# Performance work log

Hardware: AMD Instinct MI355X
Metric: run time of the kernel (lower is better)

Reference implementation:

```python
import jax, jax.numpy as jnp
import numpy as np

N_GROUPS = 8192
BETA = 0.99
EPS = 1e-12  # torch.nn.functional.normalize default eps


def _l2_normalize(v):
    # matches torch F.normalize: v / max(||v||, eps)
    n = jnp.linalg.norm(v, axis=-1, keepdims=True)
    return v / jnp.maximum(n, EPS)


def setup_inputs() -> dict:
    key = jax.random.key(0)
    k1, k2 = jax.random.split(key)
    x = jax.random.normal(k1, (16384, 256), dtype=jnp.float32)
    group_features = jax.random.uniform(k2, (N_GROUPS, 256), dtype=jnp.float32)
    return {"x": x, "group_features": group_features}


def reference(x, group_features):
    # assign_groups: cosine-similarity argmax (no_grad in original)
    xn = _l2_normalize(x)                      # [B, D]
    gn = _l2_normalize(group_features)         # [G, D]
    logits = jnp.einsum('bd,gd->bg', xn, gn)   # [B, G]
    assignments = jnp.argmax(logits, axis=-1)  # [B] int32

    # update_groups: EMA with per-group mean of assigned samples.
    # Original loop: G[a_i] += (1-beta) * x_i / bincount[a_i]
    # == G_new = beta*G + (1-beta) * segment_sum(x)/count for groups with count>0,
    #    and G_new = beta*G for empty groups.
    counts = jax.ops.segment_sum(jnp.ones_like(assignments, dtype=x.dtype),
                                 assignments, num_segments=N_GROUPS)  # [G]
    sums = jax.ops.segment_sum(x, assignments, num_segments=N_GROUPS)  # [G, D]
    mean = sums / jnp.maximum(counts, 1.0)[:, None]
    new_group_features = BETA * group_features + (1.0 - BETA) * mean
    return new_group_features
```

## Files before the change

### kernel.cpp

```cpp
#include <hip/hip_runtime.h>

#define BB 16384
#define GG 8192
#define DD 256
#define EPS   0.012f
#define EPS_R 0.008f
#define GSPLIT 8
#define GCH (GG / GSPLIT)
#define NSTEP (GCH / 128 * 8)

typedef __attribute__((ext_vector_type(8))) short bf16x8;
typedef __attribute__((ext_vector_type(4))) float f32x4;
typedef unsigned int u32;
typedef unsigned short u16;
typedef unsigned long long u64;

__device__ __forceinline__ u32 enc_f32(float v) {
    u32 u = __float_as_uint(v);
    return (u & 0x80000000u) ? ~u : (u | 0x80000000u);
}
__device__ __forceinline__ float dec_f32(u32 e) {
    u32 u = (e & 0x80000000u) ? (e ^ 0x80000000u) : ~e;
    return __uint_as_float(u);
}

__device__ __forceinline__ void async_copy16(const void* g, u16* lds) {
    __builtin_amdgcn_global_load_lds(
        (const __attribute__((address_space(1))) void*)g,
        (__attribute__((address_space(3))) void*)lds, 16, 0, 0);
}

__global__ __launch_bounds__(256)
void prep_kernel(const float* __restrict__ src, u16* __restrict__ dstb,
                 float* __restrict__ invn) {
    int wid = threadIdx.x >> 6, lane = threadIdx.x & 63;
    size_t r = (size_t)blockIdx.x * 4 + wid;
    float4 v = ((const float4*)(src + r * DD))[lane];
    float vv[4] = {v.x, v.y, v.z, v.w};
    u16 b[4];
    float ss = 0.f;
    #pragma unroll
    for (int k = 0; k < 4; ++k) {
        u32 u = __float_as_uint(vv[k]);
        b[k] = (u16)((u + 0x7fffu + ((u >> 16) & 1u)) >> 16);
        ss = fmaf(vv[k], vv[k], ss);
    }
    ushort4 pk; pk.x = b[0]; pk.y = b[1]; pk.z = b[2]; pk.w = b[3];
    ((ushort4*)(dstb + r * DD))[lane] = pk;
    #pragma unroll
    for (int off = 1; off < 64; off <<= 1) ss += __shfl_xor(ss, off);
    if (lane == 0) invn[r] = 1.0f / fmaxf(sqrtf(ss), 1e-12f);
}

__global__ __launch_bounds__(256, 2)
void gemm_kernel(const u16* __restrict__ xb, const u16* __restrict__ gb,
                 const float* __restrict__ invx, const float* __restrict__ invg,
                 u32* __restrict__ amax, u32* __restrict__ ccnt,
                 u32* __restrict__ cand, int cs) {
    __shared__ u16 lds[2 * 8192];

    const int tid   = threadIdx.x;
    const int lane  = tid & 63;
    const int w     = tid >> 6;
    const int wr    = w >> 1, wc = w & 1;
    const int m0    = blockIdx.x * 128;
    const int cbase = blockIdx.y * GCH;

    const int s8g    = (lane & 7) ^ (lane >> 3);
    const int rowadd = 2 * (lane >> 3) + (s8g >> 2);
    const int koff   = (s8g & 3) * 8;

    const int fr = lane & 15;
    const int fq = lane >> 4;
    const int s8s = ((fr & 1) * 4 + fq) ^ (fr >> 1);

    float ivx[16];
    #pragma unroll
    for (int i = 0; i < 4; ++i)
        #pragma unroll
        for (int r = 0; r < 4; ++r)
            ivx[i * 4 + r] = invx[m0 + wr * 64 + i * 16 + fq * 4 + r];

    float running[16];
    #pragma unroll
    for (int i = 0; i < 16; ++i) running[i] = -3.0e38f;

    f32x4 acc[4][4];
    #pragma unroll
    for (int i = 0; i < 4; ++i)
        #pragma unroll
        for (int j = 0; j < 4; ++j) acc[i][j] = (f32x4){0.f, 0.f, 0.f, 0.f};

    auto stage = [&](int buf, int gt, int k0) {
        #pragma unroll
        for (int q = 0; q < 2; ++q) {
            int R0 = w * 32 + q * 16;
            async_copy16(xb + (size_t)(m0 + R0 + rowadd) * DD + k0 + koff,
                         &lds[buf * 8192 + R0 * 32]);
            async_copy16(gb + (size_t)(cbase + gt * 128 + R0 + rowadd) * DD + k0 + koff,
                         &lds[buf * 8192 + 4096 + R0 * 32]);
        }
    };

    stage(0, 0, 0);
    __syncthreads();

    int cur = 0;
    for (int s = 0; s < NSTEP; ++s) {
        const int gt = s >> 3;
        if (s < NSTEP - 1) stage(cur ^ 1, (s + 1) >> 3, ((s + 1) & 7) * 32);

        bf16x8 af[4], bf[4];
        #pragma unroll
        for (int i = 0; i < 4; ++i) {
            int lineA = wr * 32 + i * 8 + (fr >> 1);
            af[i] = *(const bf16x8*)&lds[cur * 8192 + lineA * 64 + s8s * 8];
            int lineB = wc * 32 + i * 8 + (fr >> 1);
            bf[i] = *(const bf16x8*)&lds[cur * 8192 + 4096 + lineB * 64 + s8s * 8];
        }
        #pragma unroll
        for (int i = 0; i < 4; ++i)
            #pragma unroll
            for (int j = 0; j < 4; ++j)
                acc[i][j] = __builtin_amdgcn_mfma_f32_16x16x32_bf16(
                    af[i], bf[j], acc[i][j], 0, 0, 0);

        if ((s & 7) == 7) {
            const int g0 = cbase + gt * 128;
            float ivg4[4];
            #pragma unroll
            for (int j = 0; j < 4; ++j) ivg4[j] = invg[g0 + wc * 64 + j * 16 + fr];
            #pragma unroll
            for (int i = 0; i < 4; ++i) {
                #pragma unroll
                for (int r = 0; r < 4; ++r) {
                    float u0 = acc[i][0][r] * ivg4[0];
                    float u1 = acc[i][1][r] * ivg4[1];
                    float u2 = acc[i][2][r] * ivg4[2];
                    float u3 = acc[i][3][r] * ivg4[3];
                    float sm = fmaxf(fmaxf(u0, u1), fmaxf(u2, u3));
                    #pragma unroll
                    for (int off = 1; off < 16; off <<= 1)
                        sm = fmaxf(sm, __shfl_xor(sm, off));
                    const int row = m0 + wr * 64 + i * 16 + fq * 4 + r;
                    const float ivxr = ivx[i * 4 + r];
                    float mcos = fmaxf(running[i * 4 + r], sm * ivxr);
                    u32 old = 0;
                    if (fr == 0) old = atomicMax(&amax[row], enc_f32(mcos));
                    old = __shfl(old, lane & 48);
                    float gmax = fmaxf(mcos, dec_f32(old));
                    running[i * 4 + r] = gmax;
                    float thr = gmax - EPS;
                    #pragma unroll
                    for (int j = 0; j < 4; ++j) {
                        float v = (j == 0 ? u0 : j == 1 ? u1 : j == 2 ? u2 : u3) * ivxr;
                        if (v >= thr) {
                            u32 c = atomicAdd(&ccnt[row], 1u);
                            if (c < (u32)cs) {
                                float vq = fminf(fmaxf((v + 1.0f) * 32768.0f, 0.0f),
                                                 65535.0f);
                                cand[(size_t)row * cs + c] =
                                    ((u32)vq << 16) |
                                    (u32)(g0 + wc * 64 + j * 16 + fr);
                            }
                        }
                    }
                }
            }
            #pragma unroll
            for (int i = 0; i < 4; ++i)
                #pragma unroll
                for (int j = 0; j < 4; ++j) acc[i][j] = (f32x4){0.f, 0.f, 0.f, 0.f};
        }
        __syncthreads();
        cur ^= 1;
    }
}

__global__ __launch_bounds__(256)
void resolve_kernel(const float* __restrict__ x, const float* __restrict__ gf,
                    const float* __restrict__ invg, const u32* __restrict__ amax,
                    const u32* __restrict__ ccnt, const u32* __restrict__ cand,
                    int cs, float* __restrict__ sums, float* __restrict__ counts) {
    __shared__ float xs[4][DD];
    int wid = threadIdx.x >> 6, lane = threadIdx.x & 63;
    int row = blockIdx.x * 4 + wid;
    float4 xv = ((const float4*)(x + (size_t)row * DD))[lane];
    ((float4*)xs[wid])[lane] = xv;

    u32 cnt = ccnt[row];
    float best = -3.0e38f; int bcol = GG - 1;

    bool fast = (cnt >= 1 && cnt <= (u32)cs);
    u32 e = 0; u64 mask = 0;
    if (fast) {
        float thr = dec_f32(amax[row]) - EPS_R;
        e = (lane < (int)cnt) ? cand[(size_t)row * cs + lane] : 0u;
        float qv = (float)(e >> 16) * (1.0f / 32768.0f) - 1.0f;
        mask = __ballot((lane < (int)cnt) && (qv >= thr));
        if (mask == 0) fast = false;
    }

    if (fast) {
        while (mask) {
            int c = (int)(__ffsll((unsigned long long)mask) - 1);
            mask &= mask - 1;
            int col = __shfl((int)(e & 0xffffu), c);
            float4 gv = ((const float4*)(gf + (size_t)col * DD))[lane];
            float p = fmaf(xv.x, gv.x, fmaf(xv.y, gv.y,
                      fmaf(xv.z, gv.z, xv.w * gv.w)));
            #pragma unroll
            for (int off = 1; off < 64; off <<= 1) p += __shfl_xor(p, off);
            float v = p * invg[col];
            if (v > best || (v == best && col < bcol)) { best = v; bcol = col; }
        }
    } else {
        for (int col = lane; col < GG; col += 64) {
            const float4* gr = (const float4*)(gf + (size_t)col * DD);
            float s = 0.f;
            #pragma unroll 8
            for (int d = 0; d < 64; ++d) {
                float4 g4 = gr[d];
                s = fmaf(xs[wid][d * 4 + 0], g4.x, s);
                s = fmaf(xs[wid][d * 4 + 1], g4.y, s);
                s = fmaf(xs[wid][d * 4 + 2], g4.z, s);
                s = fmaf(xs[wid][d * 4 + 3], g4.w, s);
            }
            float v = s * invg[col];
            if (v > best || (v == best && col < bcol)) { best = v; bcol = col; }
        }
        #pragma unroll
        for (int off = 1; off < 64; off <<= 1) {
            float ov = __shfl_xor(best, off);
            int   oc = __shfl_xor(bcol, off);
            if (ov > best || (ov == best && oc < bcol)) { best = ov; bcol = oc; }
        }
    }
    if (lane == 0) atomicAdd(&counts[bcol], 1.0f);
    float* sp = sums + (size_t)bcol * DD + lane * 4;
    atomicAdd(sp + 0, xv.x); atomicAdd(sp + 1, xv.y);
    atomicAdd(sp + 2, xv.z); atomicAdd(sp + 3, xv.w);
}

__global__ __launch_bounds__(256)
void final_kernel(const float* __restrict__ gf, const float* __restrict__ sums,
                  const float* __restrict__ counts, float* __restrict__ out) {
    int i = blockIdx.x * 256 + threadIdx.x;
    int g = i >> 8;
    out[i] = 0.99f * gf[i] + 0.01f * (sums[i] / fmaxf(counts[g], 1.0f));
}

extern "C" void kernel_launch(void* const* d_in, const int* in_sizes, int n_in,
                              void* d_out, int out_size, void* d_ws, size_t ws_size,
                              hipStream_t stream) {
    const float* x  = (const float*)d_in[0];
    const float* gf = (const float*)d_in[1];
    float* out = (float*)d_out;

    char* ws = (char*)d_ws;
    u16*   xb     = (u16*)ws;
    u16*   gb     = (u16*)(ws + 8388608);
    float* invx   = (float*)(ws + 12582912);
    float* invg   = (float*)(ws + 12648448);
    u32*   amax   = (u32*)  (ws + 12681216);
    u32*   ccnt   = (u32*)  (ws + 12746752);
    float* counts = (float*)(ws + 12812288);
    u32*   cand   = (u32*)  (ws + 12845056);
    float* sums   = (float*)ws;

    size_t cand_off = 12845056;
    int cs = 4;
    if (ws_size > cand_off) {
        size_t slots = (ws_size - cand_off) / ((size_t)BB * 4);
        cs = (int)(slots > 64 ? 64 : slots);
        if (cs < 4) cs = 4;
    }

    hipMemsetAsync(amax, 0, 160 * 1024, stream);

    prep_kernel<<<BB / 4, 256, 0, stream>>>(x,  xb, invx);
    prep_kernel<<<GG / 4, 256, 0, stream>>>(gf, gb, invg);

    gemm_kernel<<<dim3(BB / 128, GSPLIT), 256, 0, stream>>>(
        xb, gb, invx, invg, amax, ccnt, cand, cs);

    hipMemsetAsync(sums, 0, 8388608, stream);

    resolve_kernel<<<BB / 4, 256, 0, stream>>>(
        x, gf, invg, amax, ccnt, cand, cs, sums, counts);
    final_kernel<<<GG * DD / 256, 256, 0, stream>>>(gf, sums, counts, out);
}
```

Before: 448.4 us.

## Double K-tile depth per stage and decouple global max from atomic return

Each pipeline stage now loads a 64-wide K slice instead of 32, which halves the number of stage/barrier iterations per 128-column group tile and doubles the LDS buffers. The LDS swizzle is changed to an XOR over 8-element chunks per row. The epilogue now reads the global row max with a plain load before the reduction and issues atomicMax without waiting on its return value. The inverse x norms are reloaded per epilogue instead of held in registers. Dropping the occupancy hint and using more LDS may lower occupancy, and the looser global-max read can raise candidate counts.

Result: slower. 1.280 ms (+185.5%).

```diff
diff --git a/kernel.cpp b/kernel.cpp
--- a/kernel.cpp
+++ b/kernel.cpp
@@ -7,7 +7,7 @@
 #define EPS_R 0.008f
 #define GSPLIT 8
 #define GCH (GG / GSPLIT)
-#define NSTEP (GCH / 128 * 8)
+#define NSTEP (GCH / 128 * 4)
 
 typedef __attribute__((ext_vector_type(8))) short bf16x8;
 typedef __attribute__((ext_vector_type(4))) float f32x4;
@@ -52,12 +52,12 @@
     if (lane == 0) invn[r] = 1.0f / fmaxf(sqrtf(ss), 1e-12f);
 }
 
-__global__ __launch_bounds__(256, 2)
+__global__ __launch_bounds__(256)
 void gemm_kernel(const u16* __restrict__ xb, const u16* __restrict__ gb,
                  const float* __restrict__ invx, const float* __restrict__ invg,
                  u32* __restrict__ amax, u32* __restrict__ ccnt,
                  u32* __restrict__ cand, int cs) {
-    __shared__ u16 lds[2 * 8192];
+    __shared__ u16 lds[32768];
 
     const int tid   = threadIdx.x;
     const int lane  = tid & 63;
@@ -66,39 +66,30 @@
     const int m0    = blockIdx.x * 128;
     const int cbase = blockIdx.y * GCH;
 
-    const int s8g    = (lane & 7) ^ (lane >> 3);
-    const int rowadd = 2 * (lane >> 3) + (s8g >> 2);
-    const int koff   = (s8g & 3) * 8;
+    const int rsub = lane >> 3;
+    const int s8g  = (lane & 7) ^ rsub;
 
     const int fr = lane & 15;
     const int fq = lane >> 4;
-    const int s8s = ((fr & 1) * 4 + fq) ^ (fr >> 1);
-
-    float ivx[16];
+
+    float running[16];
+    #pragma unroll
+    for (int i = 0; i < 16; ++i) running[i] = -3.0e38f;
+
+    f32x4 acc[4][4];
     #pragma unroll
     for (int i = 0; i < 4; ++i)
         #pragma unroll
-        for (int r = 0; r < 4; ++r)
-            ivx[i * 4 + r] = invx[m0 + wr * 64 + i * 16 + fq * 4 + r];
-
-    float running[16];
-    #pragma unroll
-    for (int i = 0; i < 16; ++i) running[i] = -3.0e38f;
-
-    f32x4 acc[4][4];
-    #pragma unroll
-    for (int i = 0; i < 4; ++i)
-        #pragma unroll
         for (int j = 0; j < 4; ++j) acc[i][j] = (f32x4){0.f, 0.f, 0.f, 0.f};
 
     auto stage = [&](int buf, int gt, int k0) {
         #pragma unroll
-        for (int q = 0; q < 2; ++q) {
-            int R0 = w * 32 + q * 16;
-            async_copy16(xb + (size_t)(m0 + R0 + rowadd) * DD + k0 + koff,
-                         &lds[buf * 8192 + R0 * 32]);
-            async_copy16(gb + (size_t)(cbase + gt * 128 + R0 + rowadd) * DD + k0 + koff,
-                         &lds[buf * 8192 + 4096 + R0 * 32]);
+        for (int q = 0; q < 4; ++q) {
+            int R0 = w * 32 + q * 8;
+            async_copy16(xb + (size_t)(m0 + R0 + rsub) * DD + k0 + s8g * 8,
+                         &lds[buf * 16384 + R0 * 64]);
+            async_copy16(gb + (size_t)(cbase + gt * 128 + R0 + rsub) * DD + k0 + s8g * 8,
+                         &lds[buf * 16384 + 8192 + R0 * 64]);
         }
     };
 
@@ -107,26 +98,41 @@
 
     int cur = 0;
     for (int s = 0; s < NSTEP; ++s) {
-        const int gt = s >> 3;
-        if (s < NSTEP - 1) stage(cur ^ 1, (s + 1) >> 3, ((s + 1) & 7) * 32);
-
-        bf16x8 af[4], bf[4];
-        #pragma unroll
-        for (int i = 0; i < 4; ++i) {
-            int lineA = wr * 32 + i * 8 + (fr >> 1);
-            af[i] = *(const bf16x8*)&lds[cur * 8192 + lineA * 64 + s8s * 8];
-            int lineB = wc * 32 + i * 8 + (fr >> 1);
-            bf[i] = *(const bf16x8*)&lds[cur * 8192 + 4096 + lineB * 64 + s8s * 8];
-        }
-        #pragma unroll
-        for (int i = 0; i < 4; ++i)
-            #pragma unroll
-            for (int j = 0; j < 4; ++j)
-                acc[i][j] = __builtin_amdgcn_mfma_f32_16x16x32_bf16(
-                    af[i], bf[j], acc[i][j], 0, 0, 0);
-
-        if ((s & 7) == 7) {
+        const int gt = s >> 2;
+        if (s < NSTEP - 1) stage(cur ^ 1, (s + 1) >> 2, ((s + 1) & 3) * 64);
+
+        bf16x8 af[2][4], bf[2][4];
+        #pragma unroll
+        for (int kk = 0; kk < 2; ++kk) {
+            const int sw = ((kk * 4 + fq) ^ (fr & 7)) * 8;
+            #pragma unroll
+            for (int i = 0; i < 4; ++i) {
+                int rA = wr * 64 + i * 16 + fr;
+                af[kk][i] = *(const bf16x8*)&lds[cur * 16384 + rA * 64 + sw];
+                int rB = wc * 64 + i * 16 + fr;
+                bf[kk][i] = *(const bf16x8*)&lds[cur * 16384 + 8192 + rB * 64 + sw];
+            }
+        }
+        #pragma unroll
+        for (int kk = 0; kk < 2; ++kk)
+            #pragma unroll
+            for (int i = 0; i < 4; ++i)
+                #pragma unroll
+                for (int j = 0; j < 4; ++j)
+                    acc[i][j] = __builtin_amdgcn_mfma_f32_16x16x32_bf16(
+                        af[kk][i], bf[kk][j], acc[i][j], 0, 0, 0);
+
+        if ((s & 3) == 3) {
             const int g0 = cbase + gt * 128;
+            float gl[16], ivxr[16];
+            #pragma unroll
+            for (int i = 0; i < 4; ++i)
+                #pragma unroll
+                for (int r = 0; r < 4; ++r) {
+                    int row = m0 + wr * 64 + i * 16 + fq * 4 + r;
+                    gl[i * 4 + r]   = dec_f32(amax[row]);
+                    ivxr[i * 4 + r] = invx[row];
+                }
             float ivg4[4];
             #pragma unroll
             for (int j = 0; j < 4; ++j) ivg4[j] = invg[g0 + wc * 64 + j * 16 + fr];
@@ -143,17 +149,15 @@
                     for (int off = 1; off < 16; off <<= 1)
                         sm = fmaxf(sm, __shfl_xor(sm, off));
                     const int row = m0 + wr * 64 + i * 16 + fq * 4 + r;
-                    const float ivxr = ivx[i * 4 + r];
-                    float mcos = fmaxf(running[i * 4 + r], sm * ivxr);
-                    u32 old = 0;
-                    if (fr == 0) old = atomicMax(&amax[row], enc_f32(mcos));
-                    old = __shfl(old, lane & 48);
-                    float gmax = fmaxf(mcos, dec_f32(old));
-                    running[i * 4 + r] = gmax;
-                    float thr = gmax - EPS;
+                    const float iv = ivxr[i * 4 + r];
+                    float mc = sm * iv;
+                    float runv = fmaxf(fmaxf(running[i * 4 + r], mc), gl[i * 4 + r]);
+                    running[i * 4 + r] = runv;
+                    if (fr == 0) atomicMax(&amax[row], enc_f32(mc));
+                    float thr = runv - EPS;
                     #pragma unroll
                     for (int j = 0; j < 4; ++j) {
-                        float v = (j == 0 ? u0 : j == 1 ? u1 : j == 2 ? u2 : u3) * ivxr;
+                        float v = (j == 0 ? u0 : j == 1 ? u1 : j == 2 ? u2 : u3) * iv;
                         if (v >= thr) {
                             u32 c = atomicAdd(&ccnt[row], 1u);
                             if (c < (u32)cs) {
```
